# Kernel optimization log

Hardware: AMD Instinct MI355X
Metric: run time of the kernel (lower is better)

Reference implementation:

```python
import jax, jax.numpy as jnp
import numpy as np

N, E, F_IN = 100000, 3200000, 512
H1, D1, C = 8, 8, 16  # layer1 heads, per-head dim; layer2 out classes
NEG_SLOPE = 0.2


def _segment_softmax(e, dst, num_segments):
    # numerically-stable softmax over edges grouped by destination node
    m = jax.ops.segment_max(e, dst, num_segments=num_segments)
    ex = jnp.exp(e - m[dst])
    s = jax.ops.segment_sum(ex, dst, num_segments=num_segments)
    return ex / (s[dst] + 1e-16)


def _gat_layer(x, src, dst, W, a_src, a_dst, heads, d_out):
    n = x.shape[0]
    h = (x @ W).reshape(n, heads, d_out)          # [N,H,D]
    al_s = jnp.einsum('nhd,hd->nh', h, a_src)     # [N,H]
    al_d = jnp.einsum('nhd,hd->nh', h, a_dst)
    e = jax.nn.leaky_relu(al_s[src] + al_d[dst], NEG_SLOPE)  # [E,H]
    alpha = _segment_softmax(e, dst, n)           # [E,H]
    msg = h[src] * alpha[..., None]               # [E,H,D]
    return jax.ops.segment_sum(msg, dst, num_segments=n)  # [N,H,D]


def setup_inputs() -> dict:
    key = jax.random.key(0)
    ks = jax.random.split(key, 8)
    x = jax.random.normal(ks[0], (N, F_IN), dtype=jnp.float32)
    edge_index = jax.random.randint(ks[1], (2, E), 0, N, dtype=jnp.int64)
    W1 = jax.random.normal(ks[2], (F_IN, H1 * D1), dtype=jnp.float32) * (1.0 / np.sqrt(F_IN))
    a1_src = jax.random.normal(ks[3], (H1, D1), dtype=jnp.float32)
    a1_dst = jax.random.normal(ks[4], (H1, D1), dtype=jnp.float32)
    W2 = jax.random.normal(ks[5], (H1 * D1, C), dtype=jnp.float32) * (1.0 / np.sqrt(H1 * D1))
    a2_src = jax.random.normal(ks[6], (1, C), dtype=jnp.float32)
    a2_dst = jax.random.normal(ks[7], (1, C), dtype=jnp.float32)
    return {'x': x, 'edge_index': edge_index, 'W1': W1, 'a1_src': a1_src,
            'a1_dst': a1_dst, 'W2': W2, 'a2_src': a2_src, 'a2_dst': a2_dst}


def reference(x, edge_index, W1, a1_src, a1_dst, W2, a2_src, a2_dst):
    src, dst = edge_index[0], edge_index[1]
    # layer 1: 8 heads, concat, then ELU (dropout is identity in eval mode)
    h1 = _gat_layer(x, src, dst, W1, a1_src, a1_dst, H1, D1)  # [N,H1,D1]
    h1 = jax.nn.elu(h1.reshape(N, H1 * D1))                   # [N,64]
    # layer 2: single head -> class logits
    h2 = _gat_layer(h1, src, dst, W2, a2_src, a2_dst, 1, C)   # [N,1,C]
    return jax.nn.log_softmax(h2.reshape(N, C), axis=1)
```

## Files before the change

kernel.cpp:

```cpp
#include <hip/hip_runtime.h>
#include <math.h>

#define NEG 0.2f
#define NB 64
#define BCAP 128

typedef __attribute__((ext_vector_type(8))) short bf16x8;
typedef __attribute__((ext_vector_type(4))) float f32x4;
typedef unsigned long long ull;

static __device__ __forceinline__ float lrelu(float x){ return x > 0.f ? x : NEG*x; }

static __device__ __forceinline__ void bsplit(float v, unsigned int& hi, unsigned int& lo){
  unsigned int u = __float_as_uint(v);
  unsigned int hb = (u + 0x7fffu + ((u >> 16) & 1u)) & 0xffff0000u;
  float hf = __uint_as_float(hb);
  float l = v - hf;
  unsigned int ul = __float_as_uint(l);
  hi = hb >> 16;
  lo = (ul + 0x7fffu + ((ul >> 16) & 1u)) >> 16;
}

static __device__ __forceinline__ float bf2f(unsigned short u){
  return __uint_as_float(((unsigned int)u) << 16);
}
static __device__ __forceinline__ unsigned short f2bf(float v){
  unsigned int u = __float_as_uint(v);
  return (unsigned short)((u + 0x7fffu + ((u >> 16) & 1u)) >> 16);
}

static __device__ __forceinline__ void split8(float4 v0, float4 v1, bf16x8& h, bf16x8& l){
  float vv[8] = {v0.x, v0.y, v0.z, v0.w, v1.x, v1.y, v1.z, v1.w};
  #pragma unroll
  for (int i = 0; i < 8; ++i) {
    unsigned int hi, lo;
    bsplit(vv[i], hi, lo);
    h[i] = (short)hi;
    l[i] = (short)lo;
  }
}

__global__ void k_zero(int* __restrict__ p, int n){
  int i = blockIdx.x*blockDim.x + threadIdx.x;
  if (i < n) p[i] = 0;
}

__global__ void k_flag(const int* __restrict__ u, int* __restrict__ flag){
  if (threadIdx.x == 0 && blockIdx.x == 0) {
    int z = 1;
    for (int e = 0; e < 64; ++e) if (u[2*e+1] != 0) { z = 0; break; }
    *flag = z;
  }
}

__global__ __launch_bounds__(256) void k_part(const int* __restrict__ u,
    const int* __restrict__ flag, int* __restrict__ pcur,
    ull* __restrict__ part, int E, int n, int SEGCAP){
  __shared__ ull buf[NB][BCAP];
  __shared__ int bcnt[NB];
  __shared__ int binc[NB];
  __shared__ int bbase;
  __shared__ int nflush;
  __shared__ unsigned char flist[NB];
  const bool f = (*flag) != 0;
  const int tid = threadIdx.x;
  const int g = blockIdx.x & 7;
  if (tid < NB) bcnt[tid] = 0;
  const long long stride = (long long)gridDim.x * 256;
  const long long iters = ((long long)E + stride - 1) / stride;
  long long e = (long long)blockIdx.x*256 + tid;
  for (long long it = 0; it < iters; ++it, e += stride) {
    if (tid < NB) binc[tid] = 0;
    if (tid == 0) nflush = 0;
    __syncthreads();
    int src = 0, dst = 0, b = 0;
    const bool valid = (e < E);
    if (valid) {
      src = f ? u[2*e] : u[e];
      dst = f ? u[2*(E+e)] : u[E+e];
      b = (int)(((long long)dst * NB) / n);
      atomicAdd(&binc[b], 1);
    }
    __syncthreads();
    if (tid < NB && bcnt[tid] > 0 && bcnt[tid] + binc[tid] > BCAP) {
      int i = atomicAdd(&nflush, 1);
      flist[i] = (unsigned char)tid;
    }
    __syncthreads();
    for (int i = 0; i < nflush; ++i) {
      int b2 = flist[i];
      int c = bcnt[b2]; if (c > BCAP) c = BCAP;
      if (tid == 0) bbase = atomicAdd(&pcur[(b2*8+g)*16], c);
      __syncthreads();
      int base = bbase;
      for (int j = tid; j < c; j += 256) {
        int pos = base + j;
        if (pos < SEGCAP) part[(size_t)(b2*8+g)*SEGCAP + pos] = buf[b2][j];
      }
      __syncthreads();
      if (tid == 0) bcnt[b2] = 0;
      __syncthreads();
    }
    if (valid) {
      int pos = atomicAdd(&bcnt[b], 1);
      if (pos < BCAP) buf[b][pos] = (ull)(unsigned)src | ((ull)(unsigned)dst << 32);
    }
    __syncthreads();
  }
  for (int b2 = 0; b2 < NB; ++b2) {
    int c = bcnt[b2]; if (c > BCAP) c = BCAP;
    if (c > 0) {
      if (tid == 0) bbase = atomicAdd(&pcur[(b2*8+g)*16], c);
      __syncthreads();
      int base = bbase;
      for (int j = tid; j < c; j += 256) {
        int pos = base + j;
        if (pos < SEGCAP) part[(size_t)(b2*8+g)*SEGCAP + pos] = buf[b2][j];
      }
    }
    __syncthreads();
  }
}

__global__ __launch_bounds__(1024) void k_histL(const int* __restrict__ pcur,
    const ull* __restrict__ part, int* __restrict__ cnt, int n, int SEGCAP){
  __shared__ int lcnt[1664];
  const int b = blockIdx.x;
  const int lo = (int)(((long long)b * n + NB - 1) / NB);
  const int hi = (int)(((long long)(b+1) * n + NB - 1) / NB);
  const int m = hi - lo;
  for (int i = threadIdx.x; i < m; i += 1024) lcnt[i] = 0;
  __syncthreads();
  for (int g = 0; g < 8; ++g) {
    int s = b*8 + g;
    int c = pcur[s*16]; if (c > SEGCAP) c = SEGCAP;
    for (int i = threadIdx.x; i < c; i += 1024) {
      ull v = __builtin_nontemporal_load(&part[(size_t)s*SEGCAP + i]);
      atomicAdd(&lcnt[(int)(unsigned)(v >> 32) - lo], 1);
    }
  }
  __syncthreads();
  for (int i = threadIdx.x; i < m; i += 1024) cnt[lo + i] = lcnt[i];
}

__global__ __launch_bounds__(256) void k_scan1(const int* __restrict__ cnt,
    int* __restrict__ ro, int* __restrict__ bsum, int n){
  int t = threadIdx.x;
  int base = blockIdx.x*1024 + t*4;
  int v0 = (base+0 < n) ? cnt[base+0] : 0;
  int v1 = (base+1 < n) ? cnt[base+1] : 0;
  int v2 = (base+2 < n) ? cnt[base+2] : 0;
  int v3 = (base+3 < n) ? cnt[base+3] : 0;
  int s = v0+v1+v2+v3;
  int lane = t & 63, w = t >> 6;
  int inc = s;
  for (int off = 1; off < 64; off <<= 1) {
    int tm = __shfl_up(inc, off);
    if (lane >= off) inc += tm;
  }
  __shared__ int wsum[4];
  if (lane == 63) wsum[w] = inc;
  __syncthreads();
  int wpre = 0;
  for (int k = 0; k < 4; ++k) if (k < w) wpre += wsum[k];
  int run = wpre + inc - s;
  if (base+0 < n) ro[base+0] = run; run += v0;
  if (base+1 < n) ro[base+1] = run; run += v1;
  if (base+2 < n) ro[base+2] = run; run += v2;
  if (base+3 < n) ro[base+3] = run; run += v3;
  if (t == 255) bsum[blockIdx.x] = run;
}

__global__ void k_scan2(int* __restrict__ bsum, int nb){
  int lane = threadIdx.x;
  int carry = 0;
  for (int b = 0; b < nb; b += 64) {
    int i = b + lane;
    int v = (i < nb) ? bsum[i] : 0;
    int inc = v;
    for (int off = 1; off < 64; off <<= 1) {
      int t = __shfl_up(inc, off);
      if (lane >= off) inc += t;
    }
    if (i < nb) bsum[i] = carry + inc - v;
    carry += __shfl(inc, 63);
  }
}

__global__ void k_scan3(int* __restrict__ ro, const int* __restrict__ bsum,
                        int n, int E){
  int i = blockIdx.x*blockDim.x + threadIdx.x;
  if (i < n) ro[i] = ro[i] + bsum[i >> 10];
  if (i == 0) ro[n] = E;
}

__global__ __launch_bounds__(1024) void k_fillL(const int* __restrict__ pcur,
    const ull* __restrict__ part, const int* __restrict__ ro,
    int* __restrict__ csr, int n, int SEGCAP){
  __shared__ int lcur[1664];
  const int b = blockIdx.x;
  const int lo = (int)(((long long)b * n + NB - 1) / NB);
  const int hi = (int)(((long long)(b+1) * n + NB - 1) / NB);
  const int m = hi - lo;
  for (int i = threadIdx.x; i < m; i += 1024) lcur[i] = ro[lo + i];
  __syncthreads();
  for (int g = 0; g < 8; ++g) {
    int s = b*8 + g;
    int c = pcur[s*16]; if (c > SEGCAP) c = SEGCAP;
    for (int i = threadIdx.x; i < c; i += 1024) {
      ull v = __builtin_nontemporal_load(&part[(size_t)s*SEGCAP + i]);
      int src = (int)(unsigned)v;
      int dst = (int)(unsigned)(v >> 32);
      int p = atomicAdd(&lcur[dst - lo], 1);
      csr[p] = src;
    }
  }
}

__global__ void k_wprep(const float* __restrict__ W1, unsigned short* __restrict__ wtH,
                        unsigned short* __restrict__ wtL){
  int i = blockIdx.x*256 + threadIdx.x;
  if (i >= 512*64) return;
  int k = i >> 6, c = i & 63;
  unsigned int hi, lo;
  bsplit(W1[i], hi, lo);
  wtH[c*512 + k] = (unsigned short)hi;
  wtL[c*512 + k] = (unsigned short)lo;
}

__global__ __launch_bounds__(256) void k_proj1(const float* __restrict__ x,
    const unsigned short* __restrict__ wtH, const unsigned short* __restrict__ wtL,
    const float* __restrict__ a1s_g, const float* __restrict__ a1d_g,
    unsigned short* __restrict__ h1bf, float* __restrict__ al1s, float* __restrict__ al1d, int n){
  __shared__ float xs[128*64];
  const int tid = threadIdx.x;
  const int lane = tid & 63;
  const int w = tid >> 6;
  const int l16 = lane & 15;
  const int lhi = lane >> 4;
  const int n0 = blockIdx.x*128;
  const int r0 = n0 + w*32;

  float as_c[4], ad_c[4];
  #pragma unroll
  for (int f = 0; f < 4; ++f) { as_c[f] = a1s_g[16*f + l16]; ad_c[f] = a1d_g[16*f + l16]; }

  f32x4 acc[2][4];
  #pragma unroll
  for (int m = 0; m < 2; ++m)
    #pragma unroll
    for (int f = 0; f < 4; ++f) acc[m][f] = (f32x4){0.f,0.f,0.f,0.f};

  const unsigned short* wHp = wtH + (size_t)l16*512 + 8*lhi;
  const unsigned short* wLp = wtL + (size_t)l16*512 + 8*lhi;

  const int srow = w*32 + (lane >> 4);
  int g_row = n0 + srow;
  const int chunk = (lane & 15);

  float4 ld[8];
  #pragma unroll
  for (int i = 0; i < 8; ++i) {
    int row = n0 + srow + i*4; if (row >= n) row = n - 1;
    ld[i] = *(const float4*)(x + (size_t)row*512 + chunk*4);
  }

  for (int ks = 0; ks < 8; ++ks) {
    const int k0 = ks*64;
    #pragma unroll
    for (int i = 0; i < 8; ++i) {
      int lr = srow + i*4;
      int slot = chunk ^ (lr & 15);
      *(float4*)&xs[lr*64 + slot*4] = ld[i];
    }
    __syncthreads();
    if (ks < 7) {
      #pragma unroll
      for (int i = 0; i < 8; ++i) {
        int row = n0 + srow + i*4; if (row >= n) row = n - 1;
        ld[i] = *(const float4*)(x + (size_t)row*512 + (k0 + 64) + chunk*4);
      }
    }
    #pragma unroll
    for (int kk = 0; kk < 64; kk += 32) {
      bf16x8 bh[4], bl[4];
      #pragma unroll
      for (int f = 0; f < 4; ++f) {
        bh[f] = *(const bf16x8*)(wHp + (size_t)f*8192 + k0 + kk);
        bl[f] = *(const bf16x8*)(wLp + (size_t)f*8192 + k0 + kk);
      }
      #pragma unroll
      for (int m = 0; m < 2; ++m) {
        int lr = w*32 + 16*m + l16;
        int s0 = (kk >> 2) + 2*lhi;
        float4 v0 = *(const float4*)&xs[lr*64 + ((s0 ^ (lr & 15)) << 2)];
        float4 v1 = *(const float4*)&xs[lr*64 + (((s0 + 1) ^ (lr & 15)) << 2)];
        bf16x8 ah, al_;
        split8(v0, v1, ah, al_);
        #pragma unroll
        for (int f = 0; f < 4; ++f) {
          acc[m][f] = __builtin_amdgcn_mfma_f32_16x16x32_bf16(ah,  bh[f], acc[m][f], 0, 0, 0);
          acc[m][f] = __builtin_amdgcn_mfma_f32_16x16x32_bf16(ah,  bl[f], acc[m][f], 0, 0, 0);
          acc[m][f] = __builtin_amdgcn_mfma_f32_16x16x32_bf16(al_, bh[f], acc[m][f], 0, 0, 0);
        }
      }
    }
    __syncthreads();
  }

  #pragma unroll
  for (int m = 0; m < 2; ++m) {
    #pragma unroll
    for (int r = 0; r < 4; ++r) {
      int node = r0 + 16*m + 4*lhi + r;
      bool ok = (node < n);
      #pragma unroll
      for (int f = 0; f < 4; ++f) {
        float v = acc[m][f][r];
        if (ok) h1bf[(size_t)node*64 + 16*f + l16] = f2bf(v);
        float vs = v * as_c[f], vd = v * ad_c[f];
        vs += __shfl_xor(vs, 1); vs += __shfl_xor(vs, 2); vs += __shfl_xor(vs, 4);
        vd += __shfl_xor(vd, 1); vd += __shfl_xor(vd, 2); vd += __shfl_xor(vd, 4);
        if (ok && (l16 & 7) == 0) {
          int head = 2*f + (l16 >> 3);
          al1s[node*8 + head] = vs;
          al1d[node*8 + head] = vd;
        }
      }
    }
  }
}

__global__ __launch_bounds__(256) void k_agg1(const int* __restrict__ ro,
    const int* __restrict__ csr, const float* __restrict__ al1s,
    const float* __restrict__ al1d, const unsigned short* __restrict__ h1bf,
    float* __restrict__ h1b, int n){
  int wid = blockIdx.x*4 + (threadIdx.x >> 6);
  if (wid >= n) return;
  int node = __builtin_amdgcn_readfirstlane(wid);
  int lane = threadIdx.x & 63;
  int h = lane >> 3;
  int beg = ro[node], end = ro[node+1];
  float ald = al1d[node*8 + h];
  float s = 0.f, acc = 0.f;
  if (beg < end) {
    int   srcb[4];
    float alb[4], hvb[4];
    #pragma unroll
    for (int j = 0; j < 4; ++j) {
      int idx = beg + j;
      srcb[j] = csr[idx < end ? idx : beg];
    }
    #pragma unroll
    for (int j = 0; j < 4; ++j) {
      alb[j] = al1s[srcb[j]*8 + h];
      hvb[j] = bf2f(h1bf[(size_t)srcb[j]*64 + lane]);
    }
    for (int t = beg; t < end; t += 4) {
      int   nsrc[4];
      float nal[4], nhv[4];
      #pragma unroll
      for (int j = 0; j < 4; ++j) {
        int idx = t + 4 + j;
        nsrc[j] = csr[idx < end ? idx : beg];
      }
      #pragma unroll
      for (int j = 0; j < 4; ++j) {
        nal[j] = al1s[nsrc[j]*8 + h];
        nhv[j] = bf2f(h1bf[(size_t)nsrc[j]*64 + lane]);
      }
      #pragma unroll
      for (int j = 0; j < 4; ++j) {
        float e = alb[j] + ald;
        e = e > 0.f ? e : NEG*e;
        float ex = (t + j < end) ? __expf(e) : 0.f;
        s += ex;
        acc = fmaf(hvb[j], ex, acc);
      }
      #pragma unroll
      for (int j = 0; j < 4; ++j) { srcb[j] = nsrc[j]; alb[j] = nal[j]; hvb[j] = nhv[j]; }
    }
  }
  float v = acc / (s + 1e-16f);
  v = v > 0.f ? v : expm1f(v);
  h1b[(size_t)node*64 + lane] = v;
}

__global__ __launch_bounds__(256) void k_proj2(const float* __restrict__ h1b,
    const float* __restrict__ W2, const float* __restrict__ a2s_g, const float* __restrict__ a2d_g,
    unsigned short* __restrict__ h2bf, float* __restrict__ al2s, float* __restrict__ al2d, int n){
  __shared__ float w[64*16];
  __shared__ float a2sv[16], a2dv[16];
  for (int i = threadIdx.x; i < 1024; i += 256) w[i] = W2[i];
  if (threadIdx.x < 16) { a2sv[threadIdx.x] = a2s_g[threadIdx.x]; a2dv[threadIdx.x] = a2d_g[threadIdx.x]; }
  __syncthreads();
  int c = threadIdx.x & 15;
  int nid = blockIdx.x*16 + (threadIdx.x >> 4);
  if (nid >= n) return;
  const float* row = h1b + (size_t)nid*64;
  float acc = 0.f;
  #pragma unroll
  for (int k0 = 0; k0 < 64; k0 += 4) {
    float4 r = *(const float4*)(row + k0);
    acc = fmaf(r.x, w[(k0+0)*16 + c], acc);
    acc = fmaf(r.y, w[(k0+1)*16 + c], acc);
    acc = fmaf(r.z, w[(k0+2)*16 + c], acc);
    acc = fmaf(r.w, w[(k0+3)*16 + c], acc);
  }
  h2bf[(size_t)nid*16 + c] = f2bf(acc);
  float vs = acc * a2sv[c], vd = acc * a2dv[c];
  vs += __shfl_xor(vs, 1); vs += __shfl_xor(vs, 2); vs += __shfl_xor(vs, 4); vs += __shfl_xor(vs, 8);
  vd += __shfl_xor(vd, 1); vd += __shfl_xor(vd, 2); vd += __shfl_xor(vd, 4); vd += __shfl_xor(vd, 8);
  if (c == 0) { al2s[nid] = vs; al2d[nid] = vd; }
}

__global__ __launch_bounds__(256) void k_agg2(const int* __restrict__ ro,
    const int* __restrict__ csr, const float* __restrict__ al2s,
    const float* __restrict__ al2d, const unsigned short* __restrict__ h2bf,
    float* __restrict__ out, int n){
  int wid = blockIdx.x*4 + (threadIdx.x >> 6);
  if (wid >= n) return;
  int node = __builtin_amdgcn_readfirstlane(wid);
  int lane = threadIdx.x & 63;
  int j = lane >> 4, c = lane & 15;
  int beg = ro[node], end = ro[node+1];
  float ald = al2d[node];
  float sp = 0.f, acc = 0.f;
  if (beg < end) {
    int i = beg + j;
    int sA = csr[i < end ? i : beg];
    float aA = al2s[sA];
    float hA = bf2f(h2bf[(size_t)sA*16 + c]);
    for (; i < end; i += 4) {
      int i2 = i + 4;
      int sB = csr[i2 < end ? i2 : beg];
      float aB = al2s[sB];
      float hB = bf2f(h2bf[(size_t)sB*16 + c]);
      float e = lrelu(aA + ald);
      float ex = __expf(e);
      sp += ex;
      acc = fmaf(ex, hA, acc);
      sA = sB; aA = aB; hA = hB;
    }
  }
  sp  += __shfl_xor(sp, 16);  sp  += __shfl_xor(sp, 32);
  acc += __shfl_xor(acc, 16); acc += __shfl_xor(acc, 32);
  float v = acc / (sp + 1e-16f);
  float mx = v;
  mx = fmaxf(mx, __shfl_xor(mx, 1)); mx = fmaxf(mx, __shfl_xor(mx, 2));
  mx = fmaxf(mx, __shfl_xor(mx, 4)); mx = fmaxf(mx, __shfl_xor(mx, 8));
  float l = v - mx;
  float se = __expf(l);
  se += __shfl_xor(se, 1); se += __shfl_xor(se, 2);
  se += __shfl_xor(se, 4); se += __shfl_xor(se, 8);
  float res = l - logf(se);
  if (j == 0) out[(size_t)node*16 + c] = res;
}

static inline size_t alignup(size_t x){ return (x + 255) & ~(size_t)255; }

extern "C" void kernel_launch(void* const* d_in, const int* in_sizes, int n_in,
                              void* d_out, int out_size, void* d_ws, size_t ws_size,
                              hipStream_t stream){
  const float* x   = (const float*)d_in[0];
  const int*   ei  = (const int*)  d_in[1];
  const float* W1  = (const float*)d_in[2];
  const float* a1s = (const float*)d_in[3];
  const float* a1d = (const float*)d_in[4];
  const float* W2  = (const float*)d_in[5];
  const float* a2s = (const float*)d_in[6];
  const float* a2d = (const float*)d_in[7];
  float* out = (float*)d_out;

  const int n = in_sizes[0] / 512;
  const int E = in_sizes[1] / 2;

  char* w = (char*)d_ws;
  unsigned short* h1bf = (unsigned short*)w; w += alignup((size_t)n*64*2);
  float* h1b  = (float*)w; w += alignup((size_t)n*64*4);
  float* al1s_ = (float*)w; w += alignup((size_t)n*8*4);
  float* al1d_ = (float*)w; w += alignup((size_t)n*8*4);
  unsigned short* h2bf = (unsigned short*)w; w += alignup((size_t)n*16*2);
  float* al2s_ = (float*)w; w += alignup((size_t)n*4);
  float* al2d_ = (float*)w; w += alignup((size_t)n*4);
  int* cnt    = (int*)w;   w += alignup((size_t)n*4);
  int* ro     = (int*)w;   w += alignup((size_t)(n+1)*4);
  int* csr    = (int*)w;   w += alignup((size_t)E*4);
  int* bsum   = (int*)w;   w += alignup(512*4);
  int* flag   = (int*)w;   w += alignup(64);
  int* pcur   = (int*)w;   w += alignup((size_t)NB*8*16*4);
  unsigned short* wtH = (unsigned short*)w; w += alignup(512*64*2);
  unsigned short* wtL = (unsigned short*)w; w += alignup(512*64*2);

  ull* part = (ull*)h1bf;
  const int SEGCAP = 9300;

  const int nb_scan = (n + 1023) / 1024;

  k_zero<<<(NB*8*16 + 255)/256, 256, 0, stream>>>(pcur, NB*8*16);
  k_flag<<<1, 64, 0, stream>>>(ei, flag);
  k_wprep<<<128, 256, 0, stream>>>(W1, wtH, wtL);
  k_part<<<1024, 256, 0, stream>>>(ei, flag, pcur, part, E, n, SEGCAP);
  k_histL<<<NB, 1024, 0, stream>>>(pcur, part, cnt, n, SEGCAP);
  k_scan1<<<nb_scan, 256, 0, stream>>>(cnt, ro, bsum, n);
  k_scan2<<<1, 64, 0, stream>>>(bsum, nb_scan);
  k_scan3<<<(n+255)/256, 256, 0, stream>>>(ro, bsum, n, E);
  k_fillL<<<NB, 1024, 0, stream>>>(pcur, part, ro, csr, n, SEGCAP);

  k_proj1<<<(n+127)/128, 256, 0, stream>>>(x, wtH, wtL, a1s, a1d, h1bf, al1s_, al1d_, n);
  k_agg1<<<(n+3)/4, 256, 0, stream>>>(ro, csr, al1s_, al1d_, h1bf, h1b, n);
  k_proj2<<<(n+15)/16, 256, 0, stream>>>(h1b, W2, a2s, a2d, h2bf, al2s_, al2d_, n);
  k_agg2<<<(n+3)/4, 256, 0, stream>>>(ro, csr, al2s_, al2d_, h2bf, out, n);
}
```

Measured before the change: 561.5 us.

## Double-buffer x tile via direct global-to-LDS loads in layer-1 projection

Replaces the register-staged x loads and LDS stores in the layer-1 projection GEMM with global_load_lds DMA into a double-buffered shared tile. The next k-slice is prefetched while the current one feeds the MFMAs, and the block-wide barriers are replaced by vmcnt waits, since each wave only reads rows it loaded itself. W fragments for both halves of the k-slice are also hoisted ahead of the compute. This aims to cut register pressure and LDS store overhead and to overlap memory with compute. In exchange it doubles LDS use, which may lower occupancy, and correctness depends on wave-local ownership of rows and on the vmcnt count being right.

```diff
diff --git a/kernel.cpp b/kernel.cpp
--- a/kernel.cpp
+++ b/kernel.cpp
@@ -232,7 +232,7 @@
     const unsigned short* __restrict__ wtH, const unsigned short* __restrict__ wtL,
     const float* __restrict__ a1s_g, const float* __restrict__ a1d_g,
     unsigned short* __restrict__ h1bf, float* __restrict__ al1s, float* __restrict__ al1d, int n){
-  __shared__ float xs[128*64];
+  __shared__ float xs[2][128*64];
   const int tid = threadIdx.x;
   const int lane = tid & 63;
   const int w = tid >> 6;
@@ -254,59 +254,60 @@
   const unsigned short* wHp = wtH + (size_t)l16*512 + 8*lhi;
   const unsigned short* wLp = wtL + (size_t)l16*512 + 8*lhi;
 
-  const int srow = w*32 + (lane >> 4);
-  int g_row = n0 + srow;
-  const int chunk = (lane & 15);
-
-  float4 ld[8];
+  #define STAGE(BUF, K0)                                                       \
+    _Pragma("unroll")                                                          \
+    for (int i = 0; i < 8; ++i) {                                              \
+      int lr = w*32 + i*4 + (lane >> 4);                                       \
+      int grow = n0 + lr; if (grow >= n) grow = n - 1;                         \
+      int cg = (lane & 15) ^ (lr & 15);                                        \
+      const float* gp = x + (size_t)grow*512 + (K0) + cg*4;                    \
+      __builtin_amdgcn_global_load_lds(                                        \
+          (const __attribute__((address_space(1))) void*)gp,                   \
+          (__attribute__((address_space(3))) void*)&xs[BUF][(w*8 + i)*256],    \
+          16, 0, 0);                                                           \
+    }
+
+  STAGE(0, 0)
+
   #pragma unroll
-  for (int i = 0; i < 8; ++i) {
-    int row = n0 + srow + i*4; if (row >= n) row = n - 1;
-    ld[i] = *(const float4*)(x + (size_t)row*512 + chunk*4);
-  }
-
   for (int ks = 0; ks < 8; ++ks) {
     const int k0 = ks*64;
+    const int b = ks & 1;
+    bf16x8 bh[2][4], bl[2][4];
     #pragma unroll
-    for (int i = 0; i < 8; ++i) {
-      int lr = srow + i*4;
-      int slot = chunk ^ (lr & 15);
-      *(float4*)&xs[lr*64 + slot*4] = ld[i];
-    }
-    __syncthreads();
+    for (int h = 0; h < 2; ++h)
+      #pragma unroll
+      for (int f = 0; f < 4; ++f) {
+        bh[h][f] = *(const bf16x8*)(wHp + (size_t)f*8192 + k0 + h*32);
+        bl[h][f] = *(const bf16x8*)(wLp + (size_t)f*8192 + k0 + h*32);
+      }
     if (ks < 7) {
-      #pragma unroll
-      for (int i = 0; i < 8; ++i) {
-        int row = n0 + srow + i*4; if (row >= n) row = n - 1;
-        ld[i] = *(const float4*)(x + (size_t)row*512 + (k0 + 64) + chunk*4);
-      }
+      STAGE(b ^ 1, k0 + 64)
+      asm volatile("s_waitcnt vmcnt(8)" ::: "memory");
+    } else {
+      asm volatile("s_waitcnt vmcnt(0)" ::: "memory");
     }
     #pragma unroll
-    for (int kk = 0; kk < 64; kk += 32) {
-      bf16x8 bh[4], bl[4];
-      #pragma unroll
-      for (int f = 0; f < 4; ++f) {
-        bh[f] = *(const bf16x8*)(wHp + (size_t)f*8192 + k0 + kk);
-        bl[f] = *(const bf16x8*)(wLp + (size_t)f*8192 + k0 + kk);
-      }
+    for (int h = 0; h < 2; ++h) {
+      const int kk = h*32;
       #pragma unroll
       for (int m = 0; m < 2; ++m) {
         int lr = w*32 + 16*m + l16;
-        int s0 = (kk >> 2) + 2*lhi;
-        float4 v0 = *(const float4*)&xs[lr*64 + ((s0 ^ (lr & 15)) << 2)];
-        float4 v1 = *(const float4*)&xs[lr*64 + (((s0 + 1) ^ (lr & 15)) << 2)];
+        int c0 = (kk >> 2) + 2*lhi;
+        float4 v0 = *(const float4*)&xs[b][lr*64 + ((c0 ^ l16) << 2)];
+        float4 v1 = *(const float4*)&xs[b][lr*64 + (((c0 + 1) ^ l16) << 2)];
         bf16x8 ah, al_;
         split8(v0, v1, ah, al_);
         #pragma unroll
         for (int f = 0; f < 4; ++f) {
-          acc[m][f] = __builtin_amdgcn_mfma_f32_16x16x32_bf16(ah,  bh[f], acc[m][f], 0, 0, 0);
-          acc[m][f] = __builtin_amdgcn_mfma_f32_16x16x32_bf16(ah,  bl[f], acc[m][f], 0, 0, 0);
-          acc[m][f] = __builtin_amdgcn_mfma_f32_16x16x32_bf16(al_, bh[f], acc[m][f], 0, 0, 0);
+          acc[m][f] = __builtin_amdgcn_mfma_f32_16x16x32_bf16(ah,  bh[h][f], acc[m][f], 0, 0, 0);
+          acc[m][f] = __builtin_amdgcn_mfma_f32_16x16x32_bf16(ah,  bl[h][f], acc[m][f], 0, 0, 0);
+          acc[m][f] = __builtin_amdgcn_mfma_f32_16x16x32_bf16(al_, bh[h][f], acc[m][f], 0, 0, 0);
         }
       }
     }
-    __syncthreads();
-  }
+  }
+  #undef STAGE
 
   #pragma unroll
   for (int m = 0; m < 2; ++m) {
```

New measurement: 502.5 us. 1.12x faster.
